# Kernel tuning notes

Hardware: AMD Instinct MI355X
Metric: run time of the kernel (lower is better)

The kernel has to match this reference:

```python
import jax, jax.numpy as jnp
import numpy as np

N_NODES = 100000
N_EDGES = 1600000
NODE_DIM = 128
EDGE_DIM = 64
MSG_DIM = 128
NODE_DIM_OUT = 128


def setup_inputs() -> dict:
    key = jax.random.key(0)
    k1, k2, k3, k4, k5, k6, k7 = jax.random.split(key, 7)
    node_emb = jax.random.normal(k1, (N_NODES, NODE_DIM), dtype=jnp.float32)
    edge_index = jax.random.randint(k2, (2, N_EDGES), 0, N_NODES, dtype=jnp.int64)
    edge_emb = jax.random.normal(k3, (N_EDGES, EDGE_DIM), dtype=jnp.float32)
    # Linear params (stored as [in, out]; torch uses [out, in] with x @ W.T)
    s_msg = 1.0 / np.sqrt(NODE_DIM + EDGE_DIM)
    W_msg = jax.random.uniform(k4, (NODE_DIM + EDGE_DIM, MSG_DIM), jnp.float32, -s_msg, s_msg)
    b_msg = jax.random.uniform(k5, (MSG_DIM,), jnp.float32, -s_msg, s_msg)
    s_upd = 1.0 / np.sqrt(NODE_DIM + MSG_DIM)
    W_upd = jax.random.uniform(k6, (NODE_DIM + MSG_DIM, NODE_DIM_OUT), jnp.float32, -s_upd, s_upd)
    b_upd = jax.random.uniform(k7, (NODE_DIM_OUT,), jnp.float32, -s_upd, s_upd)
    return {"node_emb": node_emb, "edge_index": edge_index, "edge_emb": edge_emb,
            "W_msg": W_msg, "b_msg": b_msg, "W_upd": W_upd, "b_upd": b_upd}


def reference(node_emb, edge_index, edge_emb, W_msg, b_msg, W_upd, b_upd):
    # PyG MessagePassing default flow: x_j = x[edge_index[0]] (source),
    # messages aggregated (mean) at edge_index[1] (target).
    src = edge_index[0]
    dst = edge_index[1]
    n = node_emb.shape[0]

    x_j = node_emb[src]                                    # [E, node_dim] gather
    msg_in = jnp.concatenate([x_j, edge_emb], axis=1)      # [E, node_dim+edge_dim]
    msg = jax.nn.relu(msg_in @ W_msg + b_msg)              # [E, msg_dim]

    # scatter-mean aggregate to nodes
    summed = jax.ops.segment_sum(msg, dst, num_segments=n)  # [N, msg_dim]
    counts = jax.ops.segment_sum(jnp.ones((msg.shape[0],), dtype=msg.dtype), dst, num_segments=n)
    mean_msg = summed / jnp.maximum(counts, 1.0)[:, None]

    upd_in = jnp.concatenate([node_emb, mean_msg], axis=1)  # [N, node_dim+msg_dim]
    h = jax.nn.relu(upd_in @ W_upd + b_upd)                 # [N, node_dim_out]
    # dropout is identity in eval mode; normalize=False (default)
    return h
```

## Files before the change

### kernel.cpp

```cpp
#include <hip/hip_runtime.h>
#include <hip/hip_bf16.h>

#define N_NODES 100000
#define N_EDGES 1600000
#define D_NODE 128
#define D_EDGE 64
#define D_MSG 128
#define K1 192
#define K2 256
#define D_OUT 128
#define NSB 98
#define TILE 64
#define NT (N_EDGES / TILE)

using frag8 = __attribute__((ext_vector_type(8))) short;
using facc  = __attribute__((ext_vector_type(4))) float;
typedef int   i32x4 __attribute__((ext_vector_type(4)));
typedef float f32x4 __attribute__((ext_vector_type(4)));
typedef float f32x2 __attribute__((ext_vector_type(2)));

static __device__ __forceinline__ unsigned short f2bf(float f) {
    unsigned int u = __float_as_uint(f);
    u = u + 0x7fffu + ((u >> 16) & 1u);
    return (unsigned short)(u >> 16);
}
static __device__ __forceinline__ float bflo(unsigned int u) { return __uint_as_float(u << 16); }
static __device__ __forceinline__ float bfhi(unsigned int u) { return __uint_as_float(u & 0xffff0000u); }

union F8 { unsigned short s[8]; frag8 f; uint4 u4; };

static __device__ __forceinline__ frag8 pack8(float4 a, float4 b) {
    F8 u;
    u.s[0] = f2bf(a.x); u.s[1] = f2bf(a.y); u.s[2] = f2bf(a.z); u.s[3] = f2bf(a.w);
    u.s[4] = f2bf(b.x); u.s[5] = f2bf(b.y); u.s[6] = f2bf(b.z); u.s[7] = f2bf(b.w);
    return u.f;
}
static __device__ __forceinline__ frag8 pack8v(f32x4 a, f32x4 b) {
    F8 u;
    u.s[0] = f2bf(a[0]); u.s[1] = f2bf(a[1]); u.s[2] = f2bf(a[2]); u.s[3] = f2bf(a[3]);
    u.s[4] = f2bf(b[0]); u.s[5] = f2bf(b[1]); u.s[6] = f2bf(b[2]); u.s[7] = f2bf(b[3]);
    return u.f;
}

__global__ void prep_all_kernel(const float* __restrict__ Wm, const float* __restrict__ Wu,
                                const float* __restrict__ node_emb, const int* __restrict__ dst,
                                unsigned short* __restrict__ WtM, unsigned short* __restrict__ WtU,
                                unsigned int* __restrict__ nodeB32, int* __restrict__ cnt) {
    int idx0 = blockIdx.x * blockDim.x + threadIdx.x;
    int stride = gridDim.x * blockDim.x;
    for (int idx = idx0; idx < 128 * K1; idx += stride) {
        int o = idx / K1, k = idx - o * K1;
        WtM[idx] = f2bf(Wm[k * D_MSG + o]);
    }
    for (int idx = idx0; idx < 128 * K2; idx += stride) {
        int o = idx >> 8, k = idx & 255;
        WtU[idx] = f2bf(Wu[k * D_OUT + o]);
    }
    const int total = N_NODES * 64;
    for (int i = idx0; i < total; i += stride) {
        float2 v = *(const float2*)&node_emb[(size_t)i * 2];
        nodeB32[i] = (unsigned)f2bf(v.x) | ((unsigned)f2bf(v.y) << 16);
    }
    for (int e = idx0; e < N_EDGES; e += stride) {
        int d = min(max(dst[e], 0), N_NODES - 1);
        atomicAdd(&cnt[d], 1);
    }
}

__global__ __launch_bounds__(1024) void scan_blocks(const int* __restrict__ cnt,
                                                    int* __restrict__ base,
                                                    int* __restrict__ part) {
    __shared__ int sh[1024];
    int i = blockIdx.x * 1024 + threadIdx.x;
    int c = (i < N_NODES) ? cnt[i] : 0;
    sh[threadIdx.x] = c;
    __syncthreads();
    for (int s = 1; s < 1024; s <<= 1) {
        int t = (threadIdx.x >= s) ? sh[threadIdx.x - s] : 0;
        __syncthreads();
        sh[threadIdx.x] += t;
        __syncthreads();
    }
    if (i < N_NODES) base[i] = sh[threadIdx.x] - c;
    if (threadIdx.x == 1023) part[blockIdx.x] = sh[1023];
}

__global__ __launch_bounds__(1024) void scan_add(int* __restrict__ base, const int* __restrict__ part) {
    __shared__ int soff;
    if (threadIdx.x < 64) {
        int l = threadIdx.x;
        int v = 0;
        if (l < blockIdx.x) v += part[l];
        if (l + 64 < blockIdx.x) v += part[l + 64];
#pragma unroll
        for (int s = 32; s; s >>= 1) v += __shfl_down(v, s, 64);
        if (l == 0) soff = v;
    }
    __syncthreads();
    int i = blockIdx.x * 1024 + threadIdx.x;
    if (i < N_NODES) base[i] += soff;
}

__global__ void scatter_kernel(const int* __restrict__ dst, const int* __restrict__ src,
                               const int* __restrict__ base, int* __restrict__ cursor,
                               i32x4* __restrict__ meta) {
    int idx0 = blockIdx.x * blockDim.x + threadIdx.x;
    int stride = gridDim.x * blockDim.x;
    for (int e = idx0; e < N_EDGES; e += stride) {
        int d = min(max(dst[e], 0), N_NODES - 1);
        int pos = base[d] + atomicAdd(&cursor[d], 1);
        i32x4 m; m[0] = e; m[1] = src[e]; m[2] = d; m[3] = 0;
        __builtin_nontemporal_store(m, &meta[pos]);
    }
}

__global__ __launch_bounds__(256, 3) void msg_fused_kernel(
    const unsigned short* __restrict__ nodeB, const i32x4* __restrict__ meta,
    const float* __restrict__ edge_emb, const unsigned short* __restrict__ WtM,
    const float* __restrict__ b_msg, const int* __restrict__ base,
    const int* __restrict__ cnt, unsigned int* __restrict__ meanB32,
    float* __restrict__ spill)
{
    __shared__ unsigned short sIn[TILE][192];
    __shared__ unsigned short sMsg[TILE][128];

    const int lane = threadIdx.x & 63;
    const int wav  = threadIdx.x >> 6;
    const int j = lane & 15;
    const int q = lane >> 4;

    frag8 wfr[2][6];
#pragma unroll
    for (int m2 = 0; m2 < 2; ++m2) {
        const unsigned short* wrow = WtM + ((wav * 2 + m2) * 16 + j) * K1;
#pragma unroll
        for (int kc = 0; kc < 6; ++kc)
            wfr[m2][kc] = *(const frag8*)&wrow[(kc * 4 + q) * 8];
    }
    float bias[2][4];
#pragma unroll
    for (int m2 = 0; m2 < 2; ++m2)
#pragma unroll
        for (int r = 0; r < 4; ++r) bias[m2][r] = b_msg[(wav * 2 + m2) * 16 + q * 4 + r];

    const int eL = threadIdx.x >> 2;
    const int qt = threadIdx.x & 3;
    const int swz = eL & 7;

    uint4 nst[4];
    f32x4 est[4];

    const int t0 = blockIdx.x;

    {
        const int e = t0 * TILE + eL;
        const i32x4 m = __builtin_nontemporal_load(&meta[e]);
        const int sp = min(max(m[1], 0), N_NODES - 1);
        const unsigned short* nrow = nodeB + (size_t)sp * D_NODE + qt * 32;
#pragma unroll
        for (int i = 0; i < 4; ++i) nst[i] = *(const uint4*)&nrow[i * 8];
        const float* erow = edge_emb + (size_t)m[0] * D_EDGE + qt * 16;
#pragma unroll
        for (int i = 0; i < 4; ++i)
            est[i] = __builtin_nontemporal_load((const f32x4*)&erow[i * 4]);
    }

#pragma unroll 1
    for (int t = t0; t < NT; t += gridDim.x) {
        const int e0 = t * TILE;

        __syncthreads();

        {
            unsigned short* drow = &sIn[eL][0];
#pragma unroll
            for (int i = 0; i < 4; ++i)
                *(uint4*)&drow[((4 * qt + i) ^ swz) * 8] = nst[i];
#pragma unroll
            for (int h = 0; h < 2; ++h) {
                F8 u;
                u.f = pack8v(est[h * 2], est[h * 2 + 1]);
                *(uint4*)&drow[((16 + 2 * qt + h) ^ swz) * 8] = u.u4;
            }
        }
        __syncthreads();

        const int tn = t + gridDim.x;
        if (tn < NT) {
            const int e = tn * TILE + eL;
            const i32x4 m = __builtin_nontemporal_load(&meta[e]);
            const int sp = min(max(m[1], 0), N_NODES - 1);
            const unsigned short* nrow = nodeB + (size_t)sp * D_NODE + qt * 32;
#pragma unroll
            for (int i = 0; i < 4; ++i) nst[i] = *(const uint4*)&nrow[i * 8];
            const float* erow = edge_emb + (size_t)m[0] * D_EDGE + qt * 16;
#pragma unroll
            for (int i = 0; i < 4; ++i)
                est[i] = __builtin_nontemporal_load((const f32x4*)&erow[i * 4]);
        }

        facc acc[2][4];
#pragma unroll
        for (int m2 = 0; m2 < 2; ++m2)
#pragma unroll
            for (int eg = 0; eg < 4; ++eg) { facc z = {0.f,0.f,0.f,0.f}; acc[m2][eg] = z; }

        const int rsw = j & 7;
#pragma unroll
        for (int eg = 0; eg < 4; ++eg) {
            const unsigned short* irow = &sIn[eg * 16 + j][0];
#pragma unroll
            for (int kc = 0; kc < 6; ++kc) {
                frag8 b = *(const frag8*)&irow[((4 * kc + q) ^ rsw) * 8];
                acc[0][eg] = __builtin_amdgcn_mfma_f32_16x16x32_bf16(wfr[0][kc], b, acc[0][eg], 0, 0, 0);
                acc[1][eg] = __builtin_amdgcn_mfma_f32_16x16x32_bf16(wfr[1][kc], b, acc[1][eg], 0, 0, 0);
            }
        }

#pragma unroll
        for (int eg = 0; eg < 4; ++eg) {
            unsigned short* mrow = &sMsg[eg * 16 + j][0];
#pragma unroll
            for (int m2 = 0; m2 < 2; ++m2) {
                float v0 = fmaxf(acc[m2][eg][0] + bias[m2][0], 0.f);
                float v1 = fmaxf(acc[m2][eg][1] + bias[m2][1], 0.f);
                float v2 = fmaxf(acc[m2][eg][2] + bias[m2][2], 0.f);
                float v3 = fmaxf(acc[m2][eg][3] + bias[m2][3], 0.f);
                uint2 w;
                w.x = (unsigned)f2bf(v0) | ((unsigned)f2bf(v1) << 16);
                w.y = (unsigned)f2bf(v2) | ((unsigned)f2bf(v3) << 16);
                int c64 = wav * 8 + m2 * 4 + q;
                *(uint2*)&mrow[(c64 ^ rsw) * 4] = w;
            }
        }
        __syncthreads();

        const int d_lo = meta[e0][2];
        const int d_hi = meta[e0 + TILE - 1][2];
        for (int n = d_lo + wav; n <= d_hi; n += 4) {
            const int b = base[n];
            const int c = cnt[n];
            const int lo = max(b - e0, 0);
            const int hi = min(b + c - e0, TILE);
            float s0 = 0.f, s1 = 0.f;
            for (int r = lo; r < hi; ++r) {
                const unsigned* mr = (const unsigned*)&sMsg[r][0];
                unsigned u = mr[(((lane >> 1) ^ (r & 7)) << 1) | (lane & 1)];
                s0 += bflo(u); s1 += bfhi(u);
            }
            const float inv = 1.0f / fmaxf((float)c, 1.0f);
            s0 *= inv; s1 *= inv;
            if (b >= e0 && b + c <= e0 + TILE) {
                unsigned int w = (unsigned)f2bf(s0) | ((unsigned)f2bf(s1) << 16);
                __builtin_nontemporal_store(w, &meanB32[(size_t)n * 64 + lane]);
            } else {
                int slot = (n == d_lo) ? 0 : 1;
                f32x2 w; w[0] = s0; w[1] = s1;
                __builtin_nontemporal_store(
                    w, (f32x2*)(spill + ((size_t)(t * 2 + slot)) * D_MSG + lane * 2));
            }
        }
    }
}

__global__ __launch_bounds__(256) void cleanup_kernel(
    const i32x4* __restrict__ meta, const int* __restrict__ base,
    const int* __restrict__ cnt, const float* __restrict__ spill,
    unsigned int* __restrict__ meanB32)
{
    const int wav = threadIdx.x >> 6;
    const int lane = threadIdx.x & 63;
    const int n = blockIdx.x * 4 + wav;
    const int c = cnt[n];
    float s0 = 0.f, s1 = 0.f;
    if (c > 0) {
        const int b = base[n];
        const int t0 = b >> 6, t1 = (b + c - 1) >> 6;
        if (t0 == t1) return;
        for (int t = t0; t <= t1; ++t) {
            const int slot = (meta[t * TILE][2] == n) ? 0 : 1;
            const float* sp = spill + ((size_t)(t * 2 + slot)) * D_MSG + lane * 2;
            s0 += sp[0]; s1 += sp[1];
        }
    }
    meanB32[(size_t)n * 64 + lane] = (unsigned)f2bf(s0) | ((unsigned)f2bf(s1) << 16);
}

__global__ __launch_bounds__(256) void node_gemm_kernel(
    const unsigned short* __restrict__ nodeB, const unsigned short* __restrict__ meanB,
    const unsigned short* __restrict__ WtU, const float* __restrict__ b_upd,
    float* __restrict__ out)
{
    __shared__ unsigned short sW[128 * K2];

    for (int idx = threadIdx.x; idx < 128 * 32; idx += 256) {
        int o = idx >> 5, ch = idx & 31;
        *(uint4*)&sW[o * K2 + (ch ^ (o & 7)) * 8] = *(const uint4*)&WtU[o * K2 + ch * 8];
    }

    const int lane = threadIdx.x & 63;
    const int wav  = threadIdx.x >> 6;
    const int j = lane & 15;
    const int q = lane >> 4;
    const int rs = j & 7;

    float bias[32];
#pragma unroll
    for (int mt = 0; mt < 8; ++mt)
#pragma unroll
        for (int r = 0; r < 4; ++r) bias[mt * 4 + r] = b_upd[mt * 16 + q * 4 + r];
    __syncthreads();

    const int n0w = blockIdx.x * 256 + wav * 64;

#pragma unroll 1
    for (int g = 0; g < 4; ++g) {
        const int n = n0w + g * 16 + j;
        const bool valid = (n < N_NODES);
        const size_t nn = valid ? (size_t)n : 0;

        frag8 bfr[8];
        const unsigned short* nrow = nodeB + nn * D_NODE;
#pragma unroll
        for (int kc = 0; kc < 4; ++kc)
            bfr[kc] = *(const frag8*)&nrow[kc * 32 + q * 8];
        const unsigned short* mrow = meanB + nn * D_MSG;
#pragma unroll
        for (int kc = 0; kc < 4; ++kc)
            bfr[4 + kc] = *(const frag8*)&mrow[kc * 32 + q * 8];

        facc acc[8];
#pragma unroll
        for (int mt = 0; mt < 8; ++mt) { facc z = {0.f, 0.f, 0.f, 0.f}; acc[mt] = z; }

#pragma unroll
        for (int mt = 0; mt < 8; ++mt) {
            const unsigned short* wrow = &sW[(mt * 16 + j) * K2];
#pragma unroll
            for (int kc = 0; kc < 8; ++kc) {
                frag8 a = *(const frag8*)&wrow[((kc * 4 + q) ^ rs) * 8];
                acc[mt] = __builtin_amdgcn_mfma_f32_16x16x32_bf16(a, bfr[kc], acc[mt], 0, 0, 0);
            }
        }

        if (valid) {
            float* orow = out + (size_t)n * D_OUT;
#pragma unroll
            for (int mt = 0; mt < 8; ++mt)
#pragma unroll
                for (int r = 0; r < 4; ++r)
                    orow[mt * 16 + q * 4 + r] = fmaxf(acc[mt][r] + bias[mt * 4 + r], 0.f);
        }
    }
}

__global__ void prep_w_kernel(const float* __restrict__ Wm, const float* __restrict__ Wu,
                              unsigned short* __restrict__ WtM, unsigned short* __restrict__ WtU) {
    int idx0 = blockIdx.x * blockDim.x + threadIdx.x;
    int stride = gridDim.x * blockDim.x;
    for (int idx = idx0; idx < 128 * K1; idx += stride) {
        int o = idx / K1, k = idx - o * K1;
        WtM[idx] = f2bf(Wm[k * D_MSG + o]);
    }
    for (int idx = idx0; idx < 128 * K2; idx += stride) {
        int o = idx >> 8, k = idx & 255;
        WtU[idx] = f2bf(Wu[k * D_OUT + o]);
    }
}

__global__ void hist_kernel(const int* __restrict__ dst, int* __restrict__ cnt) {
    int idx0 = blockIdx.x * blockDim.x + threadIdx.x;
    int stride = gridDim.x * blockDim.x;
    for (int e = idx0; e < N_EDGES; e += stride) {
        int d = min(max(dst[e], 0), N_NODES - 1);
        atomicAdd(&cnt[d], 1);
    }
}

__global__ __launch_bounds__(256) void msg_agg_kernel_fb(
    const float* __restrict__ node_emb, const i32x4* __restrict__ meta,
    const float* __restrict__ edge_emb, const unsigned short* __restrict__ WtM,
    const float* __restrict__ b_msg, const int* __restrict__ cnt,
    float* __restrict__ mean)
{
    __shared__ unsigned short sW[128 * K1];

    for (int idx = threadIdx.x; idx < 128 * 24; idx += 256) {
        int o = idx / 24, ch = idx % 24;
        *(uint4*)&sW[o * K1 + (ch ^ (o & 7)) * 8] = *(const uint4*)&WtM[o * K1 + ch * 8];
    }

    const int lane = threadIdx.x & 63;
    const int wav  = threadIdx.x >> 6;
    const int j = lane & 15;
    const int q = lane >> 4;

    float bias[32];
#pragma unroll
    for (int mt = 0; mt < 8; ++mt)
#pragma unroll
        for (int r = 0; r < 4; ++r) bias[mt * 4 + r] = b_msg[mt * 16 + q * 4 + r];
    __syncthreads();

    const int e0w = blockIdx.x * 256 + wav * 64;
    float carry[32];
    int carry_d = -1;

#pragma unroll 1
    for (int g = 0; g < 4; ++g) {
        const int e = e0w + g * 16 + j;
        const i32x4 m = meta[e];
        const int p = m[0];
        const int d = m[2];
        const int sp = min(max(m[1], 0), N_NODES - 1);
        const float invc = 1.0f / (float)cnt[d];

        frag8 bfr[6];
        const float* nrow = node_emb + (size_t)sp * D_NODE;
#pragma unroll
        for (int kc = 0; kc < 4; ++kc) {
            float4 a = *(const float4*)&nrow[kc * 32 + q * 8];
            float4 c = *(const float4*)&nrow[kc * 32 + q * 8 + 4];
            bfr[kc] = pack8(a, c);
        }
        const float* erow = edge_emb + (size_t)p * D_EDGE;
#pragma unroll
        for (int kc = 0; kc < 2; ++kc) {
            float4 a = *(const float4*)&erow[kc * 32 + q * 8];
            float4 c = *(const float4*)&erow[kc * 32 + q * 8 + 4];
            bfr[4 + kc] = pack8(a, c);
        }

        facc acc[8];
#pragma unroll
        for (int mt = 0; mt < 8; ++mt) { facc z = {0.f, 0.f, 0.f, 0.f}; acc[mt] = z; }

#pragma unroll
        for (int mt = 0; mt < 8; ++mt) {
            const unsigned short* wrow = &sW[(mt * 16 + j) * K1];
            const int rs = j & 7;
#pragma unroll
            for (int kc = 0; kc < 6; ++kc) {
                frag8 a = *(const frag8*)&wrow[((kc * 4 + q) ^ rs) * 8];
                acc[mt] = __builtin_amdgcn_mfma_f32_16x16x32_bf16(a, bfr[kc], acc[mt], 0, 0, 0);
            }
        }

        float v[32];
#pragma unroll
        for (int mt = 0; mt < 8; ++mt)
#pragma unroll
            for (int r = 0; r < 4; ++r) {
                float t = acc[mt][r] + bias[mt * 4 + r];
                v[mt * 4 + r] = fmaxf(t, 0.f) * invc;
            }

        int dprev = __shfl_up(d, 1, 16);
        int head = (j == 0 || d != dprev) ? 1 : 0;
        int seg = head;
#pragma unroll
        for (int s = 1; s < 16; s <<= 1) { int t = __shfl_up(seg, s, 16); if (j >= s) seg += t; }
        int sg1 = __shfl_up(seg, 1, 16);
        int sg2 = __shfl_up(seg, 2, 16);
        int sg4 = __shfl_up(seg, 4, 16);
        int sg8 = __shfl_up(seg, 8, 16);
        bool ok1 = (j >= 1) && (sg1 == seg);
        bool ok2 = (j >= 2) && (sg2 == seg);
        bool ok4 = (j >= 4) && (sg4 == seg);
        bool ok8 = (j >= 8) && (sg8 == seg);

#pragma unroll
        for (int i = 0; i < 32; ++i) { float t = __shfl_up(v[i], 1, 16); if (ok1) v[i] += t; }
#pragma unroll
        for (int i = 0; i < 32; ++i) { float t = __shfl_up(v[i], 2, 16); if (ok2) v[i] += t; }
#pragma unroll
        for (int i = 0; i < 32; ++i) { float t = __shfl_up(v[i], 4, 16); if (ok4) v[i] += t; }
#pragma unroll
        for (int i = 0; i < 32; ++i) { float t = __shfl_up(v[i], 8, 16); if (ok8) v[i] += t; }

        int d0 = __shfl(d, 0, 16);
        if (g > 0) {
            if (d0 != carry_d) {
                if (j == 0) {
                    float* mrow = mean + (size_t)carry_d * D_MSG;
#pragma unroll
                    for (int mt = 0; mt < 8; ++mt)
#pragma unroll
                        for (int r = 0; r < 4; ++r)
                            atomicAdd(&mrow[mt * 16 + q * 4 + r], carry[mt * 4 + r]);
                }
            } else if (seg == 1) {
#pragma unroll
                for (int i = 0; i < 32; ++i) v[i] += carry[i];
            }
        }

#pragma unroll
        for (int i = 0; i < 32; ++i) carry[i] = __shfl(v[i], 15, 16);
        carry_d = __shfl(d, 15, 16);

        int dnext = __shfl_down(d, 1, 16);
        bool tail = (j < 15) ? (dnext != d) : (g == 3);
        if (tail) {
            float* mrow = mean + (size_t)d * D_MSG;
#pragma unroll
            for (int mt = 0; mt < 8; ++mt)
#pragma unroll
                for (int r = 0; r < 4; ++r)
                    atomicAdd(&mrow[mt * 16 + q * 4 + r], v[mt * 4 + r]);
        }
    }
}

__global__ __launch_bounds__(256) void node_kernel_fb(
    const float* __restrict__ node_emb, const float* __restrict__ mean,
    const unsigned short* __restrict__ WtU, const float* __restrict__ b_upd,
    float* __restrict__ out)
{
    __shared__ unsigned short sW[128 * K2];

    for (int idx = threadIdx.x; idx < 128 * 32; idx += 256) {
        int o = idx >> 5, ch = idx & 31;
        *(uint4*)&sW[o * K2 + (ch ^ (o & 7)) * 8] = *(const uint4*)&WtU[o * K2 + ch * 8];
    }

    const int lane = threadIdx.x & 63;
    const int wav  = threadIdx.x >> 6;
    const int j = lane & 15;
    const int q = lane >> 4;

    float bias[32];
#pragma unroll
    for (int mt = 0; mt < 8; ++mt)
#pragma unroll
        for (int r = 0; r < 4; ++r) bias[mt * 4 + r] = b_upd[mt * 16 + q * 4 + r];
    __syncthreads();

    const int n0w = blockIdx.x * 256 + wav * 64;

#pragma unroll 1
    for (int g = 0; g < 4; ++g) {
        const int n = n0w + g * 16 + j;
        const bool valid = (n < N_NODES);
        const size_t nn = valid ? (size_t)n : 0;

        frag8 bfr[8];
        const float* nrow = node_emb + nn * D_NODE;
#pragma unroll
        for (int kc = 0; kc < 4; ++kc) {
            float4 a = *(const float4*)&nrow[kc * 32 + q * 8];
            float4 c = *(const float4*)&nrow[kc * 32 + q * 8 + 4];
            bfr[kc] = pack8(a, c);
        }
        const float* mrow = mean + nn * D_MSG;
#pragma unroll
        for (int kc = 0; kc < 4; ++kc) {
            float4 a = *(const float4*)&mrow[kc * 32 + q * 8];
            float4 c = *(const float4*)&mrow[kc * 32 + q * 8 + 4];
            bfr[4 + kc] = pack8(a, c);
        }

        facc acc[8];
#pragma unroll
        for (int mt = 0; mt < 8; ++mt) { facc z = {0.f, 0.f, 0.f, 0.f}; acc[mt] = z; }

#pragma unroll
        for (int mt = 0; mt < 8; ++mt) {
            const unsigned short* wrow = &sW[(mt * 16 + j) * K2];
            const int rs = j & 7;
#pragma unroll
            for (int kc = 0; kc < 8; ++kc) {
                frag8 a = *(const frag8*)&wrow[((kc * 4 + q) ^ rs) * 8];
                acc[mt] = __builtin_amdgcn_mfma_f32_16x16x32_bf16(a, bfr[kc], acc[mt], 0, 0, 0);
            }
        }

        if (valid) {
            float* orow = out + (size_t)n * D_OUT;
#pragma unroll
            for (int mt = 0; mt < 8; ++mt)
#pragma unroll
                for (int r = 0; r < 4; ++r)
                    orow[mt * 16 + q * 4 + r] = fmaxf(acc[mt][r] + bias[mt * 4 + r], 0.f);
        }
    }
}

extern "C" void kernel_launch(void* const* d_in, const int* in_sizes, int n_in,
                              void* d_out, int out_size, void* d_ws, size_t ws_size,
                              hipStream_t stream) {
    const float* node_emb = (const float*)d_in[0];
    const int*   edge_idx = (const int*)d_in[1];
    const float* edge_emb = (const float*)d_in[2];
    const float* W_msg    = (const float*)d_in[3];
    const float* b_msg    = (const float*)d_in[4];
    const float* W_upd    = (const float*)d_in[5];
    const float* b_upd    = (const float*)d_in[6];
    float* out = (float*)d_out;

    const int* src = edge_idx;
    const int* dst = edge_idx + N_EDGES;

    char* W = (char*)d_ws;

    if (ws_size >= 104000000ULL) {
        unsigned short* meanB = (unsigned short*)(W + 0);
        int* cnt     = (int*)(W + 25600000);
        int* cursor  = (int*)(W + 26000000);
        int* base    = (int*)(W + 26400000);
        int* part    = (int*)(W + 26800000);
        i32x4* meta  = (i32x4*)(W + 26800512);
        unsigned short* WtM   = (unsigned short*)(W + 52400512);
        unsigned short* WtU   = (unsigned short*)(W + 52449664);
        unsigned short* nodeB = (unsigned short*)(W + 52515200);
        float* spill = (float*)(W + 78115200);

        hipMemsetAsync(W + 25600000, 0, 800000, stream);

        prep_all_kernel<<<2048, 256, 0, stream>>>(W_msg, W_upd, node_emb, dst,
                                                  WtM, WtU, (unsigned int*)nodeB, cnt);
        scan_blocks<<<NSB, 1024, 0, stream>>>(cnt, base, part);
        scan_add<<<NSB, 1024, 0, stream>>>(base, part);
        scatter_kernel<<<1024, 256, 0, stream>>>(dst, src, base, cursor, meta);
        msg_fused_kernel<<<2048, 256, 0, stream>>>(nodeB, meta, edge_emb,
                                                   WtM, b_msg, base, cnt,
                                                   (unsigned int*)meanB, spill);
        cleanup_kernel<<<25000, 256, 0, stream>>>(meta, base, cnt, spill,
                                                  (unsigned int*)meanB);
        node_gemm_kernel<<<391, 256, 0, stream>>>(nodeB, meanB, WtU, b_upd, out);
    } else {
        float* mean  = (float*)W;
        int* cnt     = (int*)(W + 51200000);
        int* cursor  = (int*)(W + 51600000);
        int* base    = (int*)(W + 52000000);
        int* part    = (int*)(W + 52400000);
        i32x4* meta  = (i32x4*)(W + 52400512);
        unsigned short* WtM = (unsigned short*)(W + 78000512);
        unsigned short* WtU = (unsigned short*)(W + 78049664);

        hipMemsetAsync(d_ws, 0, 52000000, stream);

        prep_w_kernel<<<224, 256, 0, stream>>>(W_msg, W_upd, WtM, WtU);
        hist_kernel<<<1024, 256, 0, stream>>>(dst, cnt);
        scan_blocks<<<NSB, 1024, 0, stream>>>(cnt, base, part);
        scan_add<<<NSB, 1024, 0, stream>>>(base, part);
        scatter_kernel<<<1024, 256, 0, stream>>>(dst, src, base, cursor, meta);
        msg_agg_kernel_fb<<<6250, 256, 0, stream>>>(node_emb, meta, edge_emb, WtM,
                                                    b_msg, cnt, mean);
        node_kernel_fb<<<391, 256, 0, stream>>>(node_emb, mean, WtU, b_upd, out);
    }
}
```

Baseline: 620.2 us.

## Tune occupancy, drop nontemporal loads, grid-stride cleanup, halve node GEMM tile

Raises msg_fused_kernel launch bounds from 3 to 4 waves per SIMD and replaces nontemporal loads of meta and edge embeddings with ordinary cached loads. The cleanup kernel becomes a grid-stride loop over 1600 blocks instead of one launch covering every node, and the node GEMM processes 128 nodes per block across 782 blocks for better CU coverage. The higher occupancy target may force register spills in the fused kernel, and cached loads may evict nodeB rows that are reused from cache.

```diff
diff --git a/kernel.cpp b/kernel.cpp
--- a/kernel.cpp
+++ b/kernel.cpp
@@ -16,7 +16,6 @@
 using frag8 = __attribute__((ext_vector_type(8))) short;
 using facc  = __attribute__((ext_vector_type(4))) float;
 typedef int   i32x4 __attribute__((ext_vector_type(4)));
-typedef float f32x4 __attribute__((ext_vector_type(4)));
 typedef float f32x2 __attribute__((ext_vector_type(2)));
 
 static __device__ __forceinline__ unsigned short f2bf(float f) {
@@ -33,12 +32,6 @@
     F8 u;
     u.s[0] = f2bf(a.x); u.s[1] = f2bf(a.y); u.s[2] = f2bf(a.z); u.s[3] = f2bf(a.w);
     u.s[4] = f2bf(b.x); u.s[5] = f2bf(b.y); u.s[6] = f2bf(b.z); u.s[7] = f2bf(b.w);
-    return u.f;
-}
-static __device__ __forceinline__ frag8 pack8v(f32x4 a, f32x4 b) {
-    F8 u;
-    u.s[0] = f2bf(a[0]); u.s[1] = f2bf(a[1]); u.s[2] = f2bf(a[2]); u.s[3] = f2bf(a[3]);
-    u.s[4] = f2bf(b[0]); u.s[5] = f2bf(b[1]); u.s[6] = f2bf(b[2]); u.s[7] = f2bf(b[3]);
     return u.f;
 }
 
@@ -114,7 +107,7 @@
     }
 }
 
-__global__ __launch_bounds__(256, 3) void msg_fused_kernel(
+__global__ __launch_bounds__(256, 4) void msg_fused_kernel(
     const unsigned short* __restrict__ nodeB, const i32x4* __restrict__ meta,
     const float* __restrict__ edge_emb, const unsigned short* __restrict__ WtM,
     const float* __restrict__ b_msg, const int* __restrict__ base,
@@ -147,22 +140,21 @@
     const int qt = threadIdx.x & 3;
     const int swz = eL & 7;
 
-    uint4 nst[4];
-    f32x4 est[4];
+    uint4  nst[4];
+    float4 est[4];
 
     const int t0 = blockIdx.x;
 
     {
         const int e = t0 * TILE + eL;
-        const i32x4 m = __builtin_nontemporal_load(&meta[e]);
+        const i32x4 m = meta[e];
         const int sp = min(max(m[1], 0), N_NODES - 1);
         const unsigned short* nrow = nodeB + (size_t)sp * D_NODE + qt * 32;
 #pragma unroll
         for (int i = 0; i < 4; ++i) nst[i] = *(const uint4*)&nrow[i * 8];
         const float* erow = edge_emb + (size_t)m[0] * D_EDGE + qt * 16;
 #pragma unroll
-        for (int i = 0; i < 4; ++i)
-            est[i] = __builtin_nontemporal_load((const f32x4*)&erow[i * 4]);
+        for (int i = 0; i < 4; ++i) est[i] = *(const float4*)&erow[i * 4];
     }
 
 #pragma unroll 1
@@ -179,7 +171,7 @@
 #pragma unroll
             for (int h = 0; h < 2; ++h) {
                 F8 u;
-                u.f = pack8v(est[h * 2], est[h * 2 + 1]);
+                u.f = pack8(est[h * 2], est[h * 2 + 1]);
                 *(uint4*)&drow[((16 + 2 * qt + h) ^ swz) * 8] = u.u4;
             }
         }
@@ -188,15 +180,14 @@
         const int tn = t + gridDim.x;
         if (tn < NT) {
             const int e = tn * TILE + eL;
-            const i32x4 m = __builtin_nontemporal_load(&meta[e]);
+            const i32x4 m = meta[e];
             const int sp = min(max(m[1], 0), N_NODES - 1);
             const unsigned short* nrow = nodeB + (size_t)sp * D_NODE + qt * 32;
 #pragma unroll
             for (int i = 0; i < 4; ++i) nst[i] = *(const uint4*)&nrow[i * 8];
             const float* erow = edge_emb + (size_t)m[0] * D_EDGE + qt * 16;
 #pragma unroll
-            for (int i = 0; i < 4; ++i)
-                est[i] = __builtin_nontemporal_load((const f32x4*)&erow[i * 4]);
+            for (int i = 0; i < 4; ++i) est[i] = *(const float4*)&erow[i * 4];
         }
 
         facc acc[2][4];
@@ -235,8 +226,8 @@
         }
         __syncthreads();
 
-        const int d_lo = meta[e0][2];
-        const int d_hi = meta[e0 + TILE - 1][2];
+        const int d_lo = ((const int*)&meta[e0])[2];
+        const int d_hi = ((const int*)&meta[e0 + TILE - 1])[2];
         for (int n = d_lo + wav; n <= d_hi; n += 4) {
             const int b = base[n];
             const int c = cnt[n];
@@ -270,20 +261,22 @@
 {
     const int wav = threadIdx.x >> 6;
     const int lane = threadIdx.x & 63;
-    const int n = blockIdx.x * 4 + wav;
-    const int c = cnt[n];
-    float s0 = 0.f, s1 = 0.f;
-    if (c > 0) {
-        const int b = base[n];
-        const int t0 = b >> 6, t1 = (b + c - 1) >> 6;
-        if (t0 == t1) return;
-        for (int t = t0; t <= t1; ++t) {
-            const int slot = (meta[t * TILE][2] == n) ? 0 : 1;
-            const float* sp = spill + ((size_t)(t * 2 + slot)) * D_MSG + lane * 2;
-            s0 += sp[0]; s1 += sp[1];
-        }
-    }
-    meanB32[(size_t)n * 64 + lane] = (unsigned)f2bf(s0) | ((unsigned)f2bf(s1) << 16);
+    const int nstride = gridDim.x * 4;
+    for (int n = blockIdx.x * 4 + wav; n < N_NODES; n += nstride) {
+        const int c = cnt[n];
+        float s0 = 0.f, s1 = 0.f;
+        if (c > 0) {
+            const int b = base[n];
+            const int t0 = b >> 6, t1 = (b + c - 1) >> 6;
+            if (t0 == t1) continue;
+            for (int t = t0; t <= t1; ++t) {
+                const int slot = (((const int*)&meta[t * TILE])[2] == n) ? 0 : 1;
+                const float* sp = spill + ((size_t)(t * 2 + slot)) * D_MSG + lane * 2;
+                s0 += sp[0]; s1 += sp[1];
+            }
+        }
+        meanB32[(size_t)n * 64 + lane] = (unsigned)f2bf(s0) | ((unsigned)f2bf(s1) << 16);
+    }
 }
 
 __global__ __launch_bounds__(256) void node_gemm_kernel(
@@ -311,10 +304,10 @@
         for (int r = 0; r < 4; ++r) bias[mt * 4 + r] = b_upd[mt * 16 + q * 4 + r];
     __syncthreads();
 
-    const int n0w = blockIdx.x * 256 + wav * 64;
+    const int n0w = blockIdx.x * 128 + wav * 32;
 
 #pragma unroll 1
-    for (int g = 0; g < 4; ++g) {
+    for (int g = 0; g < 2; ++g) {
         const int n = n0w + g * 16 + j;
         const bool valid = (n < N_NODES);
         const size_t nn = valid ? (size_t)n : 0;
@@ -625,9 +618,9 @@
         msg_fused_kernel<<<2048, 256, 0, stream>>>(nodeB, meta, edge_emb,
                                                    WtM, b_msg, base, cnt,
                                                    (unsigned int*)meanB, spill);
-        cleanup_kernel<<<25000, 256, 0, stream>>>(meta, base, cnt, spill,
-                                                  (unsigned int*)meanB);
-        node_gemm_kernel<<<391, 256, 0, stream>>>(nodeB, meanB, WtU, b_upd, out);
+        cleanup_kernel<<<1600, 256, 0, stream>>>(meta, base, cnt, spill,
+                                                 (unsigned int*)meanB);
+        node_gemm_kernel<<<782, 256, 0, stream>>>(nodeB, meanB, WtU, b_upd, out);
     } else {
         float* mean  = (float*)W;
         int* cnt     = (int*)(W + 51200000);
```

New measurement: 588.8 us. 5.1% less time.
